# Optimization experiments

Measured on AMD Instinct MI355X. Metric: run time of the kernel, lower is better.

Reference implementation:

```python
import jax, jax.numpy as jnp
import numpy as np

B, L, H = 16, 512, 1024
HEADS, HEAD_SIZE = 12, 64
NEG = 1e12


def sinusoidal_position_embedding(seq_len, output_dim):
    pos = jnp.arange(seq_len, dtype=jnp.float32)[:, None]
    idx = jnp.arange(output_dim // 2, dtype=jnp.float32)
    freqs = pos * jnp.power(10000.0, -2.0 * idx / output_dim)  # [L, D/2]
    emb = jnp.stack([jnp.sin(freqs), jnp.cos(freqs)], axis=-1)  # [L, D/2, 2]
    return emb.reshape(seq_len, output_dim)  # interleaved sin/cos, [L, D]


def setup_inputs() -> dict:
    key = jax.random.key(0)
    k1, k2, k3 = jax.random.split(key, 3)
    inputs = jax.random.normal(k1, (B, L, H), dtype=jnp.float32)
    mask = jnp.ones((B, L), dtype=jnp.int32)
    W = jax.random.normal(k2, (H, HEADS * HEAD_SIZE * 2), dtype=jnp.float32) / np.sqrt(H)
    b = jax.random.normal(k3, (HEADS * HEAD_SIZE * 2,), dtype=jnp.float32) * 0.01
    pos_emb = sinusoidal_position_embedding(L, HEAD_SIZE)  # [L, HEAD_SIZE]
    return {"inputs": inputs, "mask": mask, "W": W, "b": b, "pos_emb": pos_emb}


def rotate_half_interleaved(x):
    # stack([-x[..., 1::2], x[..., ::2]], -1).reshape(x.shape)
    x2 = jnp.stack([-x[..., 1::2], x[..., ::2]], axis=-1)
    return x2.reshape(x.shape)


def reference(inputs, mask, W, b, pos_emb):
    bsz, seq_len, _ = inputs.shape
    d = pos_emb.shape[-1]
    heads = W.shape[1] // (2 * d)
    out = inputs @ W + b                       # [B, L, heads*2d]
    out = out.reshape(bsz, seq_len, heads, 2 * d)
    qw, kw = out[..., :d], out[..., d:]        # [B, L, heads, d]
    cos_pos = jnp.repeat(pos_emb[:, 1::2], 2, axis=-1)[None, :, None, :]  # [1,L,1,d]
    sin_pos = jnp.repeat(pos_emb[:, 0::2], 2, axis=-1)[None, :, None, :]
    qw = qw * cos_pos + rotate_half_interleaved(qw) * sin_pos
    kw = kw * cos_pos + rotate_half_interleaved(kw) * sin_pos
    logits = jnp.einsum('bmhd,bnhd->bhmn', qw, kw)  # [B, heads, L, L]
    pad = mask.astype(logits.dtype)[:, None, None, :] * mask.astype(logits.dtype)[:, None, :, None]
    # torch code: expand of mask[:,None,None,:] -> applies along last axis only;
    # replicate exactly: pad_mask broadcasts mask over the query axis.
    pad_mask = jnp.broadcast_to(mask.astype(logits.dtype)[:, None, None, :], logits.shape)
    logits = logits * pad_mask - (1.0 - pad_mask) * NEG
    tril = jnp.tril(jnp.ones((seq_len, seq_len), dtype=logits.dtype), -1)
    logits = logits - tril[None, None, :, :] * NEG
    return logits / jnp.sqrt(jnp.array(d, dtype=logits.dtype))
```

## Files before the change

kernel.cpp:

```cpp
#include <hip/hip_runtime.h>

#define BB 16
#define LL 512
#define HH 1024
#define HEADS 12
#define DD 64
#define N1 1536
#define M1 8192
#define NEGC 1e12f

typedef short bf16x8 __attribute__((ext_vector_type(8)));
typedef float f32x4 __attribute__((ext_vector_type(4)));

typedef const __attribute__((address_space(1))) void* as1cvp;
typedef __attribute__((address_space(3))) void* as3vp;

__device__ __forceinline__ unsigned short f2bf(float f) {
    union { float f; unsigned int u; } v; v.f = f;
    unsigned int u = v.u;
    return (unsigned short)((u + 0x7fffu + ((u >> 16) & 1u)) >> 16);
}

__device__ __forceinline__ void gl_lds16(const void* g, void* l) {
    __builtin_amdgcn_global_load_lds((as1cvp)g, (as3vp)l, 16, 0, 0);
}

__global__ __launch_bounds__(256) void k_conv_x(const float* __restrict__ X,
                                                unsigned short* __restrict__ Xb,
                                                int n4) {
    int i = blockIdx.x * 256 + threadIdx.x;
    if (i >= n4) return;
    float4 v = ((const float4*)X)[i];
    ushort4 o;
    o.x = f2bf(v.x); o.y = f2bf(v.y); o.z = f2bf(v.z); o.w = f2bf(v.w);
    ((ushort4*)Xb)[i] = o;
}

__global__ __launch_bounds__(256) void k_trans_w(const float* __restrict__ W,
                                                 unsigned short* __restrict__ Wt) {
    __shared__ float tile[32][33];
    int n0 = blockIdx.x * 32;
    int k0 = blockIdx.y * 32;
    int tx = threadIdx.x;
    int ty = threadIdx.y;
#pragma unroll
    for (int i = 0; i < 4; i++) {
        int k = ty + i * 8;
        tile[k][tx] = W[(size_t)(k0 + k) * N1 + n0 + tx];
    }
    __syncthreads();
#pragma unroll
    for (int i = 0; i < 4; i++) {
        int n = ty + i * 8;
        Wt[(size_t)(n0 + n) * HH + k0 + tx] = f2bf(tile[tx][n]);
    }
}

__global__ __launch_bounds__(256) void k_gemm1_rope(
    const unsigned short* __restrict__ Xb,
    const unsigned short* __restrict__ Wt,
    const float* __restrict__ bias,
    const float* __restrict__ pe,
    unsigned short* __restrict__ Qr,
    unsigned short* __restrict__ Kr)
{
    __shared__ __align__(16) unsigned short As[128 * 32];
    __shared__ __align__(16) unsigned short Bs[128 * 32];
    int m0 = blockIdx.y * 128;
    int n0 = blockIdx.x * 128;
    int tid = threadIdx.x;
    int w  = tid >> 6;
    int ln = tid & 63;
    int lq = ln >> 4;
    int lm = ln & 15;
    int wm = (w & 1) * 64;
    int wn = (w >> 1) * 64;

    int srow = tid >> 2;
    int scol = (tid & 3) * 8;
    const unsigned short* ga0 = &Xb[(size_t)(m0 + srow) * HH + scol];
    const unsigned short* ga1 = &Xb[(size_t)(m0 + 64 + srow) * HH + scol];
    const unsigned short* gb0 = &Wt[(size_t)(n0 + srow) * HH + scol];
    const unsigned short* gb1 = &Wt[(size_t)(n0 + 64 + srow) * HH + scol];
    unsigned short* la = &As[w * 512];
    unsigned short* lb = &Bs[w * 512];

    f32x4 acc[4][4] = {};

    for (int kk = 0; kk < HH; kk += 32) {
        gl_lds16(ga0 + kk, la);
        gl_lds16(ga1 + kk, la + 2048);
        gl_lds16(gb0 + kk, lb);
        gl_lds16(gb1 + kk, lb + 2048);
        __syncthreads();

        bf16x8 a[4], b[4];
#pragma unroll
        for (int i = 0; i < 4; i++) {
            a[i] = *(const bf16x8*)&As[(wm + i * 16 + lm) * 32 + lq * 8];
            b[i] = *(const bf16x8*)&Bs[(wn + i * 16 + lm) * 32 + lq * 8];
        }
#pragma unroll
        for (int mi = 0; mi < 4; mi++)
#pragma unroll
            for (int ni = 0; ni < 4; ni++)
                acc[mi][ni] = __builtin_amdgcn_mfma_f32_16x16x32_bf16(
                    a[mi], b[ni], acc[mi][ni], 0, 0, 0);
        __syncthreads();
    }

#pragma unroll
    for (int ni = 0; ni < 4; ni++) {
        int n = n0 + wn + ni * 16 + lm;
        float bv = bias[n];
        int h = n >> 7;
        int c = n & 127;
        int j = c & 63;
        int ii = j >> 1;
        bool isK = (c >= 64);
        unsigned short* dst = isK ? Kr : Qr;
#pragma unroll
        for (int mi = 0; mi < 4; mi++) {
#pragma unroll
            for (int r = 0; r < 4; r++) {
                int m = m0 + wm + mi * 16 + lq * 4 + r;
                int l = m & (LL - 1);
                int bidx = m >> 9;
                float v = acc[mi][ni][r] + bv;
                float vp = __shfl_xor(v, 1, 64);
                float2 sc = *(const float2*)&pe[l * 64 + 2 * ii];
                float o = (j & 1) ? (v * sc.y + vp * sc.x) : (v * sc.y - vp * sc.x);
                size_t idx = ((size_t)(bidx * HEADS + h) * LL + l) * DD + j;
                dst[idx] = f2bf(o);
            }
        }
    }
}

__global__ __launch_bounds__(256) void k_gemm2(
    const unsigned short* __restrict__ Qr,
    const unsigned short* __restrict__ Kr,
    const int* __restrict__ mask,
    float* __restrict__ out)
{
    int bh = blockIdx.z;
    int b  = bh / HEADS;
    int n0 = blockIdx.x * 64;
    int m0 = blockIdx.y * 64;
    int tid = threadIdx.x;
    int w  = tid >> 6;
    int ln = tid & 63;
    int lq = ln >> 4;
    int lm = ln & 15;
    int mw = (w & 1) * 32;
    int nw = (w >> 1) * 32;

    const unsigned short* Qb = Qr + (size_t)bh * LL * DD;
    const unsigned short* Kb = Kr + (size_t)bh * LL * DD;

    f32x4 acc[2][2] = {};
#pragma unroll
    for (int kk = 0; kk < 64; kk += 32) {
        bf16x8 q0 = *(const bf16x8*)&Qb[(size_t)(m0 + mw + lm) * DD + kk + lq * 8];
        bf16x8 q1 = *(const bf16x8*)&Qb[(size_t)(m0 + mw + 16 + lm) * DD + kk + lq * 8];
        bf16x8 k0 = *(const bf16x8*)&Kb[(size_t)(n0 + nw + lm) * DD + kk + lq * 8];
        bf16x8 k1 = *(const bf16x8*)&Kb[(size_t)(n0 + nw + 16 + lm) * DD + kk + lq * 8];
        acc[0][0] = __builtin_amdgcn_mfma_f32_16x16x32_bf16(k0, q0, acc[0][0], 0, 0, 0);
        acc[0][1] = __builtin_amdgcn_mfma_f32_16x16x32_bf16(k0, q1, acc[0][1], 0, 0, 0);
        acc[1][0] = __builtin_amdgcn_mfma_f32_16x16x32_bf16(k1, q0, acc[1][0], 0, 0, 0);
        acc[1][1] = __builtin_amdgcn_mfma_f32_16x16x32_bf16(k1, q1, acc[1][1], 0, 0, 0);
    }

#pragma unroll
    for (int nt = 0; nt < 2; nt++) {
        int nb = n0 + nw + nt * 16 + lq * 4;
        int4 mv = *(const int4*)&mask[b * LL + nb];
#pragma unroll
        for (int mt = 0; mt < 2; mt++) {
            int m = m0 + mw + mt * 16 + lm;
            f32x4 o;
#pragma unroll
            for (int r = 0; r < 4; r++) {
                int n = nb + r;
                float pm = (float)(((const int*)&mv)[r]);
                float dot = acc[nt][mt][r];
                float val = (dot * pm - (1.0f - pm) * NEGC - (n < m ? NEGC : 0.0f)) * 0.125f;
                o[r] = val;
            }
            __builtin_nontemporal_store(o, (f32x4*)&out[((size_t)bh * LL + m) * LL + nb]);
        }
    }
}

extern "C" void kernel_launch(void* const* d_in, const int* in_sizes, int n_in,
                              void* d_out, int out_size, void* d_ws, size_t ws_size,
                              hipStream_t stream) {
    const float* X    = (const float*)d_in[0];
    const int*   mask = (const int*)d_in[1];
    const float* W    = (const float*)d_in[2];
    const float* bias = (const float*)d_in[3];
    const float* pe   = (const float*)d_in[4];
    float* out = (float*)d_out;

    char* ws = (char*)d_ws;
    unsigned short* Xb = (unsigned short*)ws;
    unsigned short* Wt = (unsigned short*)(ws + 16777216);
    unsigned short* Qr = (unsigned short*)(ws + 16777216 + 3145728);
    unsigned short* Kr = Qr + (size_t)BB * HEADS * LL * DD;

    k_conv_x<<<dim3((M1 * HH / 4 + 255) / 256), dim3(256), 0, stream>>>(X, Xb, M1 * HH / 4);
    k_trans_w<<<dim3(N1 / 32, HH / 32), dim3(32, 8), 0, stream>>>(W, Wt);
    k_gemm1_rope<<<dim3(N1 / 128, M1 / 128), dim3(256), 0, stream>>>(Xb, Wt, bias, pe, Qr, Kr);
    k_gemm2<<<dim3(LL / 64, LL / 64, BB * HEADS), dim3(256), 0, stream>>>(Qr, Kr, mask, out);
}
```

Before: 322.3 us.

## Merge prep kernels, vectorize RoPE epilogue, enlarge QK tiles and skip masked tiles

```diff
diff --git a/kernel.cpp b/kernel.cpp
--- a/kernel.cpp
+++ b/kernel.cpp
@@ -25,34 +25,36 @@
     __builtin_amdgcn_global_load_lds((as1cvp)g, (as3vp)l, 16, 0, 0);
 }
 
-__global__ __launch_bounds__(256) void k_conv_x(const float* __restrict__ X,
-                                                unsigned short* __restrict__ Xb,
-                                                int n4) {
-    int i = blockIdx.x * 256 + threadIdx.x;
-    if (i >= n4) return;
-    float4 v = ((const float4*)X)[i];
-    ushort4 o;
-    o.x = f2bf(v.x); o.y = f2bf(v.y); o.z = f2bf(v.z); o.w = f2bf(v.w);
-    ((ushort4*)Xb)[i] = o;
-}
-
-__global__ __launch_bounds__(256) void k_trans_w(const float* __restrict__ W,
-                                                 unsigned short* __restrict__ Wt) {
+__global__ __launch_bounds__(256) void k_prep(const float* __restrict__ X,
+                                              unsigned short* __restrict__ Xb,
+                                              const float* __restrict__ W,
+                                              unsigned short* __restrict__ Wt) {
     __shared__ float tile[32][33];
-    int n0 = blockIdx.x * 32;
-    int k0 = blockIdx.y * 32;
-    int tx = threadIdx.x;
-    int ty = threadIdx.y;
-#pragma unroll
-    for (int i = 0; i < 4; i++) {
-        int k = ty + i * 8;
-        tile[k][tx] = W[(size_t)(k0 + k) * N1 + n0 + tx];
-    }
-    __syncthreads();
-#pragma unroll
-    for (int i = 0; i < 4; i++) {
-        int n = ty + i * 8;
-        Wt[(size_t)(n0 + n) * HH + k0 + tx] = f2bf(tile[tx][n]);
+    int blk = blockIdx.x;
+    int tid = threadIdx.x;
+    if (blk < 8192) {
+        int i = blk * 256 + tid;
+        float4 v = ((const float4*)X)[i];
+        ushort4 o;
+        o.x = f2bf(v.x); o.y = f2bf(v.y); o.z = f2bf(v.z); o.w = f2bf(v.w);
+        ((ushort4*)Xb)[i] = o;
+    } else {
+        int bi = blk - 8192;
+        int n0 = (bi % 48) * 32;
+        int k0 = (bi / 48) * 32;
+        int tx = tid & 31;
+        int ty = tid >> 5;
+#pragma unroll
+        for (int i = 0; i < 4; i++) {
+            int k = ty + i * 8;
+            tile[k][tx] = W[(size_t)(k0 + k) * N1 + n0 + tx];
+        }
+        __syncthreads();
+#pragma unroll
+        for (int i = 0; i < 4; i++) {
+            int n = ty + i * 8;
+            Wt[(size_t)(n0 + n) * HH + k0 + tx] = f2bf(tile[tx][n]);
+        }
     }
 }
 
@@ -101,38 +103,40 @@
             b[i] = *(const bf16x8*)&Bs[(wn + i * 16 + lm) * 32 + lq * 8];
         }
 #pragma unroll
-        for (int mi = 0; mi < 4; mi++)
-#pragma unroll
-            for (int ni = 0; ni < 4; ni++)
-                acc[mi][ni] = __builtin_amdgcn_mfma_f32_16x16x32_bf16(
-                    a[mi], b[ni], acc[mi][ni], 0, 0, 0);
+        for (int ni = 0; ni < 4; ni++)
+#pragma unroll
+            for (int mi = 0; mi < 4; mi++)
+                acc[ni][mi] = __builtin_amdgcn_mfma_f32_16x16x32_bf16(
+                    b[ni], a[mi], acc[ni][mi], 0, 0, 0);
         __syncthreads();
     }
 
 #pragma unroll
     for (int ni = 0; ni < 4; ni++) {
-        int n = n0 + wn + ni * 16 + lm;
-        float bv = bias[n];
-        int h = n >> 7;
-        int c = n & 127;
-        int j = c & 63;
-        int ii = j >> 1;
-        bool isK = (c >= 64);
-        unsigned short* dst = isK ? Kr : Qr;
+        int nb = n0 + wn + ni * 16 + lq * 4;
+        int h  = nb >> 7;
+        int c  = nb & 127;
+        int jb = c & 63;
+        unsigned short* dst = (c >= 64) ? Kr : Qr;
+        float4 bv = *(const float4*)&bias[nb];
 #pragma unroll
         for (int mi = 0; mi < 4; mi++) {
-#pragma unroll
-            for (int r = 0; r < 4; r++) {
-                int m = m0 + wm + mi * 16 + lq * 4 + r;
-                int l = m & (LL - 1);
-                int bidx = m >> 9;
-                float v = acc[mi][ni][r] + bv;
-                float vp = __shfl_xor(v, 1, 64);
-                float2 sc = *(const float2*)&pe[l * 64 + 2 * ii];
-                float o = (j & 1) ? (v * sc.y + vp * sc.x) : (v * sc.y - vp * sc.x);
-                size_t idx = ((size_t)(bidx * HEADS + h) * LL + l) * DD + j;
-                dst[idx] = f2bf(o);
-            }
+            int m = m0 + wm + mi * 16 + lm;
+            int l = m & (LL - 1);
+            int bidx = m >> 9;
+            float4 sc = *(const float4*)&pe[l * 64 + jb];
+            float v0 = acc[ni][mi][0] + bv.x;
+            float v1 = acc[ni][mi][1] + bv.y;
+            float v2 = acc[ni][mi][2] + bv.z;
+            float v3 = acc[ni][mi][3] + bv.w;
+            float o0 = v0 * sc.y - v1 * sc.x;
+            float o1 = v1 * sc.y + v0 * sc.x;
+            float o2 = v2 * sc.w - v3 * sc.z;
+            float o3 = v3 * sc.w + v2 * sc.z;
+            ushort4 ov;
+            ov.x = f2bf(o0); ov.y = f2bf(o1); ov.z = f2bf(o2); ov.w = f2bf(o3);
+            size_t idx = ((size_t)(bidx * HEADS + h) * LL + l) * DD + jb;
+            *(ushort4*)&dst[idx] = ov;
         }
     }
 }
@@ -145,49 +149,54 @@
 {
     int bh = blockIdx.z;
     int b  = bh / HEADS;
-    int n0 = blockIdx.x * 64;
-    int m0 = blockIdx.y * 64;
+    int n0 = blockIdx.x * 128;
+    int m0 = blockIdx.y * 128;
     int tid = threadIdx.x;
     int w  = tid >> 6;
     int ln = tid & 63;
     int lq = ln >> 4;
     int lm = ln & 15;
-    int mw = (w & 1) * 32;
-    int nw = (w >> 1) * 32;
+    int wm = (w & 1) * 64;
+    int wn = (w >> 1) * 64;
 
     const unsigned short* Qb = Qr + (size_t)bh * LL * DD;
     const unsigned short* Kb = Kr + (size_t)bh * LL * DD;
 
-    f32x4 acc[2][2] = {};
-#pragma unroll
-    for (int kk = 0; kk < 64; kk += 32) {
-        bf16x8 q0 = *(const bf16x8*)&Qb[(size_t)(m0 + mw + lm) * DD + kk + lq * 8];
-        bf16x8 q1 = *(const bf16x8*)&Qb[(size_t)(m0 + mw + 16 + lm) * DD + kk + lq * 8];
-        bf16x8 k0 = *(const bf16x8*)&Kb[(size_t)(n0 + nw + lm) * DD + kk + lq * 8];
-        bf16x8 k1 = *(const bf16x8*)&Kb[(size_t)(n0 + nw + 16 + lm) * DD + kk + lq * 8];
-        acc[0][0] = __builtin_amdgcn_mfma_f32_16x16x32_bf16(k0, q0, acc[0][0], 0, 0, 0);
-        acc[0][1] = __builtin_amdgcn_mfma_f32_16x16x32_bf16(k0, q1, acc[0][1], 0, 0, 0);
-        acc[1][0] = __builtin_amdgcn_mfma_f32_16x16x32_bf16(k1, q0, acc[1][0], 0, 0, 0);
-        acc[1][1] = __builtin_amdgcn_mfma_f32_16x16x32_bf16(k1, q1, acc[1][1], 0, 0, 0);
-    }
-
-#pragma unroll
-    for (int nt = 0; nt < 2; nt++) {
-        int nb = n0 + nw + nt * 16 + lq * 4;
+    f32x4 acc[4][4] = {};
+    if (n0 + 127 >= m0) {
+#pragma unroll
+        for (int kk = 0; kk < 64; kk += 32) {
+            bf16x8 q[4], k[4];
+#pragma unroll
+            for (int i = 0; i < 4; i++) {
+                q[i] = *(const bf16x8*)&Qb[(size_t)(m0 + wm + i * 16 + lm) * DD + kk + lq * 8];
+                k[i] = *(const bf16x8*)&Kb[(size_t)(n0 + wn + i * 16 + lm) * DD + kk + lq * 8];
+            }
+#pragma unroll
+            for (int ni = 0; ni < 4; ni++)
+#pragma unroll
+                for (int mi = 0; mi < 4; mi++)
+                    acc[ni][mi] = __builtin_amdgcn_mfma_f32_16x16x32_bf16(
+                        k[ni], q[mi], acc[ni][mi], 0, 0, 0);
+        }
+    }
+
+#pragma unroll
+    for (int ni = 0; ni < 4; ni++) {
+        int nb = n0 + wn + ni * 16 + lq * 4;
         int4 mv = *(const int4*)&mask[b * LL + nb];
 #pragma unroll
-        for (int mt = 0; mt < 2; mt++) {
-            int m = m0 + mw + mt * 16 + lm;
+        for (int mi = 0; mi < 4; mi++) {
+            int m = m0 + wm + mi * 16 + lm;
             f32x4 o;
 #pragma unroll
             for (int r = 0; r < 4; r++) {
                 int n = nb + r;
-                float pm = (float)(((const int*)&mv)[r]);
-                float dot = acc[nt][mt][r];
-                float val = (dot * pm - (1.0f - pm) * NEGC - (n < m ? NEGC : 0.0f)) * 0.125f;
-                o[r] = val;
+                float pm = (float)((&mv.x)[r]);
+                float dot = acc[ni][mi][r];
+                o[r] = (dot * pm - (1.0f - pm) * NEGC - (n < m ? NEGC : 0.0f)) * 0.125f;
             }
-            __builtin_nontemporal_store(o, (f32x4*)&out[((size_t)bh * LL + m) * LL + nb]);
+            *(f32x4*)&out[((size_t)bh * LL + m) * LL + nb] = o;
         }
     }
 }
@@ -208,8 +217,7 @@
     unsigned short* Qr = (unsigned short*)(ws + 16777216 + 3145728);
     unsigned short* Kr = Qr + (size_t)BB * HEADS * LL * DD;
 
-    k_conv_x<<<dim3((M1 * HH / 4 + 255) / 256), dim3(256), 0, stream>>>(X, Xb, M1 * HH / 4);
-    k_trans_w<<<dim3(N1 / 32, HH / 32), dim3(32, 8), 0, stream>>>(W, Wt);
+    k_prep<<<dim3(8192 + 1536), dim3(256), 0, stream>>>(X, Xb, W, Wt);
     k_gemm1_rope<<<dim3(N1 / 128, M1 / 128), dim3(256), 0, stream>>>(Xb, Wt, bias, pe, Qr, Kr);
-    k_gemm2<<<dim3(LL / 64, LL / 64, BB * HEADS), dim3(256), 0, stream>>>(Qr, Kr, mask, out);
-}
+    k_gemm2<<<dim3(LL / 128, LL / 128, BB * HEADS), dim3(256), 0, stream>>>(Qr, Kr, mask, out);
+}
```

Result: slower. 338.8 us (+5.1%).
